# Optimization experiments

Measured on AMD Instinct MI355X. Metric: run time of the kernel, lower is better.

The kernel has to match this reference:

```python
import jax, jax.numpy as jnp
import numpy as np

D_MODEL = 512
N_HEAD = 8


def setup_inputs() -> dict:
    key = jax.random.key(0)
    ks = jax.random.split(key, 9)
    s = 1.0 / np.sqrt(D_MODEL)
    inp = {
        "x": jax.random.normal(ks[0], (2, 4096, D_MODEL), dtype=jnp.float32),
        "wq": jax.random.uniform(ks[1], (D_MODEL, D_MODEL), jnp.float32, -s, s),
        "bq": jax.random.uniform(ks[2], (D_MODEL,), jnp.float32, -s, s),
        "wk": jax.random.uniform(ks[3], (D_MODEL, D_MODEL), jnp.float32, -s, s),
        "bk": jax.random.uniform(ks[4], (D_MODEL,), jnp.float32, -s, s),
        "wv": jax.random.uniform(ks[5], (D_MODEL, D_MODEL), jnp.float32, -s, s),
        "bv": jax.random.uniform(ks[6], (D_MODEL,), jnp.float32, -s, s),
        "wo": jax.random.uniform(ks[7], (D_MODEL, D_MODEL), jnp.float32, -s, s),
        "bo": jax.random.uniform(ks[8], (D_MODEL,), jnp.float32, -s, s),
    }
    return inp


def reference(x, wq, bq, wk, bk, wv, bv, wo, bo):
    B, S, D = x.shape
    H = N_HEAD
    Dh = D // H

    def split_heads(t):  # [B,S,D] -> [B,H,S,Dh]
        return t.reshape(B, S, H, Dh).transpose(0, 2, 1, 3)

    q = split_heads(x @ wq.T + bq)
    k = split_heads(x @ wk.T + bk)
    v = split_heads(x @ wv.T + bv)

    # explicit (unfused) attention, matching the torch module
    score = jnp.einsum("bhsd,bhtd->bhst", q, k) / jnp.sqrt(jnp.float32(Dh))
    attn = jax.nn.softmax(score, axis=-1)
    out = jnp.einsum("bhst,bhtd->bhsd", attn, v)  # [B,H,S,Dh]

    out = out.transpose(0, 2, 1, 3).reshape(B, S, D)
    return out @ wo.T + bo
```

## Files before the change

### kernel.cpp

```cpp
#include <hip/hip_runtime.h>
#include <math.h>

#define S_LEN 4096
#define DMODEL 512
#define NHEAD 8
#define E_ELEMS ((size_t)8192 * 512)
#define QSCALE 0.18033688f

typedef __attribute__((ext_vector_type(8))) short bf16x8;
typedef __attribute__((ext_vector_type(4))) float f32x4;
typedef __attribute__((ext_vector_type(16))) float f32x16;
typedef unsigned short u16;
typedef unsigned int u32;

__device__ __forceinline__ u16 f2bf(float f) {
    u32 u = __float_as_uint(f);
    u += 0x7FFFu + ((u >> 16) & 1u);
    return (u16)(u >> 16);
}

#define MFMA16(a, b, c) __builtin_amdgcn_mfma_f32_16x16x32_bf16((a), (b), (c), 0, 0, 0)
#define MFMA32(a, b, c) __builtin_amdgcn_mfma_f32_32x32x16_bf16((a), (b), (c), 0, 0, 0)

__global__ __launch_bounds__(256) void cvt_x(const float* __restrict__ in,
                                             u16* __restrict__ out, int n4) {
    const int i = blockIdx.x * 256 + threadIdx.x;
    if (i >= n4) return;
    const float4 v = ((const float4*)in)[i];
    uint2 hp;
    hp.x = (u32)f2bf(v.x) | ((u32)f2bf(v.y) << 16);
    hp.y = (u32)f2bf(v.z) | ((u32)f2bf(v.w) << 16);
    ((uint2*)out)[i] = hp;
}

__global__ __launch_bounds__(256) void cvt_w(
    const float* __restrict__ wq, const float* __restrict__ wk,
    const float* __restrict__ wv, const float* __restrict__ wo,
    u16* __restrict__ oq, u16* __restrict__ ok,
    u16* __restrict__ ov, u16* __restrict__ oo) {
    const int i = blockIdx.x * 256 + threadIdx.x;
    {
        const float4 v = ((const float4*)wq)[i];
        uint2 hp;
        hp.x = (u32)f2bf(v.x * QSCALE) | ((u32)f2bf(v.y * QSCALE) << 16);
        hp.y = (u32)f2bf(v.z * QSCALE) | ((u32)f2bf(v.w * QSCALE) << 16);
        ((uint2*)oq)[i] = hp;
    }
    {
        const float4 v = ((const float4*)wk)[i];
        uint2 hp;
        hp.x = (u32)f2bf(v.x) | ((u32)f2bf(v.y) << 16);
        hp.y = (u32)f2bf(v.z) | ((u32)f2bf(v.w) << 16);
        ((uint2*)ok)[i] = hp;
    }
    {
        const float4 v = ((const float4*)wv)[i];
        uint2 hp;
        hp.x = (u32)f2bf(v.x) | ((u32)f2bf(v.y) << 16);
        hp.y = (u32)f2bf(v.z) | ((u32)f2bf(v.w) << 16);
        ((uint2*)ov)[i] = hp;
    }
    {
        const float4 v = ((const float4*)wo)[i];
        uint2 hp;
        hp.x = (u32)f2bf(v.x) | ((u32)f2bf(v.y) << 16);
        hp.y = (u32)f2bf(v.z) | ((u32)f2bf(v.w) << 16);
        ((uint2*)oo)[i] = hp;
    }
}

template<int MODE>
__global__ __launch_bounds__(256) void proj_kernel(
    const u16* __restrict__ Abf,
    const u16* __restrict__ Wq, const float* __restrict__ Bq,
    const u16* __restrict__ Wk, const float* __restrict__ Bk,
    const u16* __restrict__ Wv, const float* __restrict__ Bv,
    u16* __restrict__ Qo, u16* __restrict__ Ko, u16* __restrict__ Vt,
    float* __restrict__ Out)
{
    __shared__ __align__(16) u16 sm[18432];
    u16* Ah = sm;
    u16* Bh = sm + 9216;

    const int tid = threadIdx.x;
    const int w = tid >> 6, lane = tid & 63, g = lane >> 4, c = lane & 15;
    const int bm = blockIdx.x * 128;
    const int n0 = blockIdx.y * 64;
    const int z = (MODE == 0) ? blockIdx.z : 0;
    const u16* W   = (MODE == 1) ? Wq : (z == 0 ? Wq : (z == 1 ? Wk : Wv));
    const float* Bi = (MODE == 1) ? Bq : (z == 0 ? Bq : (z == 1 ? Bk : Bv));
    const float bsc = (MODE == 0 && z == 0) ? QSCALE : 1.0f;

    f32x4 acc[2][4];
    #pragma unroll
    for (int a = 0; a < 2; ++a)
        #pragma unroll
        for (int b = 0; b < 4; ++b) acc[a][b] = (f32x4){0.f, 0.f, 0.f, 0.f};

    #pragma unroll 1
    for (int kt = 0; kt < 8; ++kt) {
        const int k0 = kt * 64;
        __syncthreads();
        #pragma unroll
        for (int i = 0; i < 4; ++i) {
            const int slot = i * 256 + tid;
            const int r = slot >> 3, c8 = slot & 7;
            *(uint4*)(Ah + r * 72 + c8 * 8) =
                *(const uint4*)(Abf + (size_t)(bm + r) * DMODEL + k0 + c8 * 8);
        }
        #pragma unroll
        for (int i = 0; i < 2; ++i) {
            const int slot = i * 256 + tid;
            const int r = slot >> 3, c8 = slot & 7;
            *(uint4*)(Bh + r * 72 + c8 * 8) =
                *(const uint4*)(W + (size_t)(n0 + r) * DMODEL + k0 + c8 * 8);
        }
        __syncthreads();

        #pragma unroll
        for (int kc = 0; kc < 2; ++kc) {
            bf16x8 a[2], b[4];
            #pragma unroll
            for (int mf = 0; mf < 2; ++mf)
                a[mf] = *(const bf16x8*)(Ah + (w * 32 + mf * 16 + c) * 72 + kc * 32 + g * 8);
            #pragma unroll
            for (int nf = 0; nf < 4; ++nf)
                b[nf] = *(const bf16x8*)(Bh + (nf * 16 + c) * 72 + kc * 32 + g * 8);
            #pragma unroll
            for (int mf = 0; mf < 2; ++mf)
                #pragma unroll
                for (int nf = 0; nf < 4; ++nf)
                    acc[mf][nf] = MFMA16(a[mf], b[nf], acc[mf][nf]);
        }
    }

    if (MODE == 0 && z == 2) {
        __syncthreads();
        float* scr = (float*)sm;
        #pragma unroll
        for (int mf = 0; mf < 2; ++mf)
            #pragma unroll
            for (int nf = 0; nf < 4; ++nf) {
                const float bias = Bi[n0 + nf * 16 + c];
                #pragma unroll
                for (int r = 0; r < 4; ++r)
                    scr[(w * 32 + mf * 16 + 4 * g + r) * 72 + nf * 16 + c] =
                        acc[mf][nf][r] + bias;
            }
        __syncthreads();
        const int d = tid & 63, sb = tid >> 6;
        const int b = bm >> 12, h = n0 >> 6;
        const size_t obase =
            ((size_t)((b * NHEAD + h) * 64 + d)) * S_LEN + (bm & (S_LEN - 1)) + sb * 32;
        u16 th[32];
        #pragma unroll
        for (int j = 0; j < 32; ++j)
            th[j] = f2bf(scr[(sb * 32 + j) * 72 + d]);
        #pragma unroll
        for (int q = 0; q < 4; ++q)
            *(uint4*)(Vt + obase + q * 8) = *(const uint4*)&th[q * 8];
        return;
    }

    #pragma unroll
    for (int mf = 0; mf < 2; ++mf)
        #pragma unroll
        for (int nf = 0; nf < 4; ++nf) {
            const int n = n0 + nf * 16 + c;
            const float bias = Bi[n] * bsc;
            #pragma unroll
            for (int r = 0; r < 4; ++r) {
                const int m = bm + w * 32 + mf * 16 + 4 * g + r;
                const float v = acc[mf][nf][r] + bias;
                if (MODE == 1) {
                    Out[(size_t)m * DMODEL + n] = v;
                } else {
                    const int b = m >> 12, s = m & (S_LEN - 1);
                    const int hh = n >> 6, dd = n & 63;
                    const size_t o = ((size_t)((b * NHEAD + hh) * S_LEN + s)) * 64 + dd;
                    if (z == 0) Qo[o] = f2bf(v);
                    else        Ko[o] = f2bf(v);
                }
            }
        }
}

__global__ __launch_bounds__(256, 4) void attn_kernel(
    const u16* __restrict__ Qb, const u16* __restrict__ Kb,
    const u16* __restrict__ Vt, float* __restrict__ Op, float* __restrict__ Lp)
{
    __shared__ __align__(16) u16 sm[16384];

    const int tid = threadIdx.x;
    const int w = tid >> 6, l = tid & 63;
    const int r0 = l & 31, hi = l >> 5;

    const int f = blockIdx.x;
    const int wg = (f & 7) * 128 + (f >> 3);
    const int bh = wg >> 6, kvh = (wg >> 5) & 1, qb = wg & 31;
    const int b = bh >> 3, h = bh & 7;

    const size_t hoff = (size_t)bh * S_LEN * 64;
    const int qw = qb * 128 + w * 32;
    const int kv0 = kvh * 2048;

    bf16x8 qf[4];
    #pragma unroll
    for (int kc = 0; kc < 4; ++kc)
        qf[kc] = *(const bf16x8*)(Qb + hoff + (size_t)(qw + r0) * 64 + kc * 16 + hi * 8);

    const int rbase = r0 * 64;
    int soff[4];
    #pragma unroll
    for (int j = 0; j < 4; ++j) soff[j] = ((2 * j + hi) ^ (r0 & 7)) * 8;

    const int srow0 = w * 16 + (l >> 3);
    const int slot  = l & 7;
    const int srow1 = srow0 + 8;
    const u16* srcK0 = Kb + hoff + (size_t)(kv0 + srow0) * 64 + ((slot ^ (srow0 & 7)) * 8);
    const u16* srcK1 = Kb + hoff + (size_t)(kv0 + srow1) * 64 + ((slot ^ (srow1 & 7)) * 8);
    const u16* srcV0 = Vt + ((size_t)bh * 64 + srow0) * S_LEN + kv0 + ((slot ^ (srow0 & 7)) * 8);
    const u16* srcV1 = Vt + ((size_t)bh * 64 + srow1) * S_LEN + kv0 + ((slot ^ (srow1 & 7)) * 8);

#define STAGE(bufb, t) do {                                                        \
        u16* kb_ = sm + (bufb) * 8192 + w * 1024;                                  \
        u16* vb_ = kb_ + 4096;                                                     \
        __builtin_amdgcn_global_load_lds(srcK0 + (size_t)(t) * 4096, kb_,       16, 0, 0); \
        __builtin_amdgcn_global_load_lds(srcK1 + (size_t)(t) * 4096, kb_ + 512, 16, 0, 0); \
        __builtin_amdgcn_global_load_lds(srcV0 + (size_t)(t) * 64,   vb_,       16, 0, 0); \
        __builtin_amdgcn_global_load_lds(srcV1 + (size_t)(t) * 64,   vb_ + 512, 16, 0, 0); \
    } while (0)

    f32x16 o0 = {0.f,0.f,0.f,0.f,0.f,0.f,0.f,0.f,0.f,0.f,0.f,0.f,0.f,0.f,0.f,0.f};
    f32x16 o1 = {0.f,0.f,0.f,0.f,0.f,0.f,0.f,0.f,0.f,0.f,0.f,0.f,0.f,0.f,0.f,0.f};
    float lsum = 0.f;

    STAGE(0, 0);
    __syncthreads();
    int buf = 0;

    #pragma unroll 1
    for (int t = 0; t < 32; ++t) {
        if (t + 1 < 32) STAGE(buf ^ 1, t + 1);

        const u16* Kb_s = sm + buf * 8192;
        const u16* Vb_s = Kb_s + 4096;

        f32x16 s0 = {0.f,0.f,0.f,0.f,0.f,0.f,0.f,0.f,0.f,0.f,0.f,0.f,0.f,0.f,0.f,0.f};
        f32x16 s1 = {0.f,0.f,0.f,0.f,0.f,0.f,0.f,0.f,0.f,0.f,0.f,0.f,0.f,0.f,0.f,0.f};
        #pragma unroll
        for (int kc = 0; kc < 4; ++kc) {
            const bf16x8 k0 = *(const bf16x8*)(Kb_s + rbase + soff[kc]);
            const bf16x8 k1 = *(const bf16x8*)(Kb_s + 2048 + rbase + soff[kc]);
            s0 = MFMA32(k0, qf[kc], s0);
            s1 = MFMA32(k1, qf[kc], s1);
        }

        bf16x8 pa[4];
        #pragma unroll
        for (int kvf = 0; kvf < 2; ++kvf) {
            float pe[16];
            #pragma unroll
            for (int r = 0; r < 16; ++r) {
                const float sv = kvf ? s1[r] : s0[r];
                pe[r] = __builtin_amdgcn_exp2f(sv);
                lsum += pe[r];
            }
            #pragma unroll
            for (int hf = 0; hf < 2; ++hf) {
                const int rb = hf * 8;
                u32 x0, y0, x1, y1;
                asm("v_cvt_pk_bf16_f32 %0, %1, %2" : "=v"(x0) : "v"(pe[rb+0]), "v"(pe[rb+1]));
                asm("v_cvt_pk_bf16_f32 %0, %1, %2" : "=v"(y0) : "v"(pe[rb+4]), "v"(pe[rb+5]));
                asm("v_cvt_pk_bf16_f32 %0, %1, %2" : "=v"(x1) : "v"(pe[rb+2]), "v"(pe[rb+3]));
                asm("v_cvt_pk_bf16_f32 %0, %1, %2" : "=v"(y1) : "v"(pe[rb+6]), "v"(pe[rb+7]));
                asm volatile("v_permlane32_swap_b32 %0, %1" : "+v"(x0), "+v"(y0));
                asm volatile("v_permlane32_swap_b32 %0, %1" : "+v"(x1), "+v"(y1));
                union { u32 u[4]; bf16x8 v; } P;
                P.u[0] = x0; P.u[1] = x1; P.u[2] = y0; P.u[3] = y1;
                pa[kvf * 2 + hf] = P.v;
            }
        }

        #pragma unroll
        for (int kvc = 0; kvc < 4; ++kvc) {
            const bf16x8 v0 = *(const bf16x8*)(Vb_s + rbase + soff[kvc]);
            const bf16x8 v1 = *(const bf16x8*)(Vb_s + 2048 + rbase + soff[kvc]);
            o0 = MFMA32(pa[kvc], v0, o0);
            o1 = MFMA32(pa[kvc], v1, o1);
        }

        __syncthreads();
        buf ^= 1;
    }
#undef STAGE

    lsum += __shfl_xor(lsum, 32);
    if (hi == 0)
        Lp[((size_t)kvh * 16 + bh) * S_LEN + qw + r0] = lsum;

    float* Ob = Op + ((size_t)kvh * 8192 + (size_t)b * S_LEN) * DMODEL;
    #pragma unroll
    for (int df = 0; df < 2; ++df) {
        #pragma unroll
        for (int r = 0; r < 16; ++r) {
            const float ov = df ? o1[r] : o0[r];
            const int q = (r & 3) + 8 * (r >> 2) + 4 * hi;
            Ob[(size_t)(qw + q) * DMODEL + h * 64 + df * 32 + r0] = ov;
        }
    }
}

__global__ __launch_bounds__(256) void combine_kernel(
    const float* __restrict__ Op, const float* __restrict__ Lp,
    u16* __restrict__ A)
{
    const int i = blockIdx.x * 256 + threadIdx.x;
    const int m = i >> 6;
    const int col = (i & 63) * 8;
    const int b = m >> 12, s = m & (S_LEN - 1), h = col >> 6;
    const float l0 = Lp[((size_t)b * 8 + h) * S_LEN + s];
    const float l1 = Lp[(size_t)16 * S_LEN + ((size_t)b * 8 + h) * S_LEN + s];
    const float inv = 1.0f / (l0 + l1);
    const size_t base0 = (size_t)m * DMODEL + col;
    const size_t base1 = (size_t)8192 * DMODEL + base0;
    const float4 a0 = *(const float4*)(Op + base0);
    const float4 a1 = *(const float4*)(Op + base0 + 4);
    const float4 c0 = *(const float4*)(Op + base1);
    const float4 c1 = *(const float4*)(Op + base1 + 4);
    u16 r[8];
    r[0] = f2bf((a0.x + c0.x) * inv);
    r[1] = f2bf((a0.y + c0.y) * inv);
    r[2] = f2bf((a0.z + c0.z) * inv);
    r[3] = f2bf((a0.w + c0.w) * inv);
    r[4] = f2bf((a1.x + c1.x) * inv);
    r[5] = f2bf((a1.y + c1.y) * inv);
    r[6] = f2bf((a1.z + c1.z) * inv);
    r[7] = f2bf((a1.w + c1.w) * inv);
    *(uint4*)(A + base0) = *(const uint4*)r;
}

extern "C" void kernel_launch(void* const* d_in, const int* in_sizes, int n_in,
                              void* d_out, int out_size, void* d_ws, size_t ws_size,
                              hipStream_t stream)
{
    const float* x  = (const float*)d_in[0];
    const float* wq = (const float*)d_in[1];
    const float* bq = (const float*)d_in[2];
    const float* wk = (const float*)d_in[3];
    const float* bk = (const float*)d_in[4];
    const float* wv = (const float*)d_in[5];
    const float* bv = (const float*)d_in[6];
    const float* wo = (const float*)d_in[7];
    const float* bo = (const float*)d_in[8];

    u16* ws = (u16*)d_ws;
    const size_t E = E_ELEMS;
    u16* xbf  = ws;
    u16* Qbf  = ws + E;
    u16* Kbf  = ws + 2 * E;
    u16* Vtbf = ws + 3 * E;
    u16* wqbf = ws + 4 * E;
    u16* wkbf = wqbf + DMODEL * DMODEL;
    u16* wvbf = wkbf + DMODEL * DMODEL;
    u16* wobf = wvbf + DMODEL * DMODEL;
    float* Opart = (float*)(ws + 4 * E + 4 * DMODEL * DMODEL);
    float* Lpart = Opart + (size_t)2 * 8192 * DMODEL;

    cvt_x<<<dim3(4096), 256, 0, stream>>>(x, xbf, (int)(E / 4));
    cvt_w<<<dim3(256), 256, 0, stream>>>(wq, wk, wv, wo, wqbf, wkbf, wvbf, wobf);

    proj_kernel<0><<<dim3(64, 8, 3), 256, 0, stream>>>(
        xbf, wqbf, bq, wkbf, bk, wvbf, bv, Qbf, Kbf, Vtbf, nullptr);

    attn_kernel<<<dim3(1024), 256, 0, stream>>>(Qbf, Kbf, Vtbf, Opart, Lpart);

    combine_kernel<<<dim3(2048), 256, 0, stream>>>(Opart, Lpart, xbf);

    proj_kernel<1><<<dim3(64, 8, 1), 256, 0, stream>>>(
        xbf, wobf, bo, nullptr, nullptr, nullptr, nullptr,
        nullptr, nullptr, nullptr, (float*)d_out);
}
```

Measured before the change: 153.7 us.

## Fuse split-KV combine into attention and retile Q/K/O projections with direct LDS loads

```diff
diff --git a/kernel.cpp b/kernel.cpp
--- a/kernel.cpp
+++ b/kernel.cpp
@@ -70,32 +70,34 @@
 }
 
 template<int MODE>
-__global__ __launch_bounds__(256) void proj_kernel(
+__global__ __launch_bounds__(256) void proj2_kernel(
     const u16* __restrict__ Abf,
-    const u16* __restrict__ Wq, const float* __restrict__ Bq,
-    const u16* __restrict__ Wk, const float* __restrict__ Bk,
-    const u16* __restrict__ Wv, const float* __restrict__ Bv,
-    u16* __restrict__ Qo, u16* __restrict__ Ko, u16* __restrict__ Vt,
-    float* __restrict__ Out)
+    const u16* __restrict__ W0, const float* __restrict__ Bi0,
+    const u16* __restrict__ W1, const float* __restrict__ Bi1,
+    u16* __restrict__ Qo, u16* __restrict__ Ko, float* __restrict__ Out)
 {
-    __shared__ __align__(16) u16 sm[18432];
-    u16* Ah = sm;
-    u16* Bh = sm + 9216;
+    __shared__ __align__(16) u16 sm[16384];
+    u16* As = sm;
+    u16* Bs = sm + 8192;
 
     const int tid = threadIdx.x;
-    const int w = tid >> 6, lane = tid & 63, g = lane >> 4, c = lane & 15;
+    const int w = tid >> 6, l = tid & 63, g = (l >> 4), c = l & 15;
+    const int wr = w >> 1, wc = w & 1;
     const int bm = blockIdx.x * 128;
-    const int n0 = blockIdx.y * 64;
+    const int n0 = blockIdx.y * 128;
     const int z = (MODE == 0) ? blockIdx.z : 0;
-    const u16* W   = (MODE == 1) ? Wq : (z == 0 ? Wq : (z == 1 ? Wk : Wv));
-    const float* Bi = (MODE == 1) ? Bq : (z == 0 ? Bq : (z == 1 ? Bk : Bv));
+    const u16* W   = z ? W1 : W0;
+    const float* Bi = z ? Bi1 : Bi0;
     const float bsc = (MODE == 0 && z == 0) ? QSCALE : 1.0f;
 
-    f32x4 acc[2][4];
-    #pragma unroll
-    for (int a = 0; a < 2; ++a)
-        #pragma unroll
-        for (int b = 0; b < 4; ++b) acc[a][b] = (f32x4){0.f, 0.f, 0.f, 0.f};
+    const int sr = l >> 3;
+    const int slot = l & 7;
+
+    f32x4 acc[4][4];
+    #pragma unroll
+    for (int i = 0; i < 4; ++i)
+        #pragma unroll
+        for (int j = 0; j < 4; ++j) acc[i][j] = (f32x4){0.f, 0.f, 0.f, 0.f};
 
     #pragma unroll 1
     for (int kt = 0; kt < 8; ++kt) {
@@ -103,74 +105,47 @@
         __syncthreads();
         #pragma unroll
         for (int i = 0; i < 4; ++i) {
-            const int slot = i * 256 + tid;
-            const int r = slot >> 3, c8 = slot & 7;
-            *(uint4*)(Ah + r * 72 + c8 * 8) =
-                *(const uint4*)(Abf + (size_t)(bm + r) * DMODEL + k0 + c8 * 8);
-        }
-        #pragma unroll
-        for (int i = 0; i < 2; ++i) {
-            const int slot = i * 256 + tid;
-            const int r = slot >> 3, c8 = slot & 7;
-            *(uint4*)(Bh + r * 72 + c8 * 8) =
-                *(const uint4*)(W + (size_t)(n0 + r) * DMODEL + k0 + c8 * 8);
+            const int row = i * 32 + w * 8 + sr;
+            const int scol = (slot ^ (row & 7)) * 8;
+            __builtin_amdgcn_global_load_lds(
+                Abf + (size_t)(bm + row) * DMODEL + k0 + scol,
+                As + (i * 32 + w * 8) * 64, 16, 0, 0);
+            __builtin_amdgcn_global_load_lds(
+                W + (size_t)(n0 + row) * DMODEL + k0 + scol,
+                Bs + (i * 32 + w * 8) * 64, 16, 0, 0);
         }
         __syncthreads();
 
         #pragma unroll
         for (int kc = 0; kc < 2; ++kc) {
-            bf16x8 a[2], b[4];
-            #pragma unroll
-            for (int mf = 0; mf < 2; ++mf)
-                a[mf] = *(const bf16x8*)(Ah + (w * 32 + mf * 16 + c) * 72 + kc * 32 + g * 8);
-            #pragma unroll
-            for (int nf = 0; nf < 4; ++nf)
-                b[nf] = *(const bf16x8*)(Bh + (nf * 16 + c) * 72 + kc * 32 + g * 8);
-            #pragma unroll
-            for (int mf = 0; mf < 2; ++mf)
+            bf16x8 a[4], b[4];
+            #pragma unroll
+            for (int mf = 0; mf < 4; ++mf) {
+                const int ra = wr * 64 + mf * 16 + c;
+                a[mf] = *(const bf16x8*)(As + ra * 64 + (((kc * 4 + g) ^ (ra & 7)) * 8));
+            }
+            #pragma unroll
+            for (int nf = 0; nf < 4; ++nf) {
+                const int rb = wc * 64 + nf * 16 + c;
+                b[nf] = *(const bf16x8*)(Bs + rb * 64 + (((kc * 4 + g) ^ (rb & 7)) * 8));
+            }
+            #pragma unroll
+            for (int mf = 0; mf < 4; ++mf)
                 #pragma unroll
                 for (int nf = 0; nf < 4; ++nf)
                     acc[mf][nf] = MFMA16(a[mf], b[nf], acc[mf][nf]);
         }
     }
 
-    if (MODE == 0 && z == 2) {
-        __syncthreads();
-        float* scr = (float*)sm;
-        #pragma unroll
-        for (int mf = 0; mf < 2; ++mf)
-            #pragma unroll
-            for (int nf = 0; nf < 4; ++nf) {
-                const float bias = Bi[n0 + nf * 16 + c];
-                #pragma unroll
-                for (int r = 0; r < 4; ++r)
-                    scr[(w * 32 + mf * 16 + 4 * g + r) * 72 + nf * 16 + c] =
-                        acc[mf][nf][r] + bias;
-            }
-        __syncthreads();
-        const int d = tid & 63, sb = tid >> 6;
-        const int b = bm >> 12, h = n0 >> 6;
-        const size_t obase =
-            ((size_t)((b * NHEAD + h) * 64 + d)) * S_LEN + (bm & (S_LEN - 1)) + sb * 32;
-        u16 th[32];
-        #pragma unroll
-        for (int j = 0; j < 32; ++j)
-            th[j] = f2bf(scr[(sb * 32 + j) * 72 + d]);
-        #pragma unroll
-        for (int q = 0; q < 4; ++q)
-            *(uint4*)(Vt + obase + q * 8) = *(const uint4*)&th[q * 8];
-        return;
-    }
-
-    #pragma unroll
-    for (int mf = 0; mf < 2; ++mf)
+    #pragma unroll
+    for (int mf = 0; mf < 4; ++mf)
         #pragma unroll
         for (int nf = 0; nf < 4; ++nf) {
-            const int n = n0 + nf * 16 + c;
+            const int n = n0 + wc * 64 + nf * 16 + c;
             const float bias = Bi[n] * bsc;
             #pragma unroll
             for (int r = 0; r < 4; ++r) {
-                const int m = bm + w * 32 + mf * 16 + 4 * g + r;
+                const int m = bm + wr * 64 + mf * 16 + 4 * g + r;
                 const float v = acc[mf][nf][r] + bias;
                 if (MODE == 1) {
                     Out[(size_t)m * DMODEL + n] = v;
@@ -185,24 +160,107 @@
         }
 }
 
-__global__ __launch_bounds__(256, 4) void attn_kernel(
+__global__ __launch_bounds__(256) void proj_v_kernel(
+    const u16* __restrict__ Abf, const u16* __restrict__ Wv,
+    const float* __restrict__ Bv, u16* __restrict__ Vt)
+{
+    __shared__ __align__(16) u16 sm[18432];
+    u16* Ah = sm;
+    u16* Bh = sm + 9216;
+
+    const int tid = threadIdx.x;
+    const int w = tid >> 6, lane = tid & 63, g = lane >> 4, c = lane & 15;
+    const int bm = blockIdx.x * 128;
+    const int n0 = blockIdx.y * 64;
+
+    f32x4 acc[2][4];
+    #pragma unroll
+    for (int a = 0; a < 2; ++a)
+        #pragma unroll
+        for (int b = 0; b < 4; ++b) acc[a][b] = (f32x4){0.f, 0.f, 0.f, 0.f};
+
+    #pragma unroll 1
+    for (int kt = 0; kt < 8; ++kt) {
+        const int k0 = kt * 64;
+        __syncthreads();
+        #pragma unroll
+        for (int i = 0; i < 4; ++i) {
+            const int slot = i * 256 + tid;
+            const int r = slot >> 3, c8 = slot & 7;
+            *(uint4*)(Ah + r * 72 + c8 * 8) =
+                *(const uint4*)(Abf + (size_t)(bm + r) * DMODEL + k0 + c8 * 8);
+        }
+        #pragma unroll
+        for (int i = 0; i < 2; ++i) {
+            const int slot = i * 256 + tid;
+            const int r = slot >> 3, c8 = slot & 7;
+            *(uint4*)(Bh + r * 72 + c8 * 8) =
+                *(const uint4*)(Wv + (size_t)(n0 + r) * DMODEL + k0 + c8 * 8);
+        }
+        __syncthreads();
+
+        #pragma unroll
+        for (int kc = 0; kc < 2; ++kc) {
+            bf16x8 a[2], b[4];
+            #pragma unroll
+            for (int mf = 0; mf < 2; ++mf)
+                a[mf] = *(const bf16x8*)(Ah + (w * 32 + mf * 16 + c) * 72 + kc * 32 + g * 8);
+            #pragma unroll
+            for (int nf = 0; nf < 4; ++nf)
+                b[nf] = *(const bf16x8*)(Bh + (nf * 16 + c) * 72 + kc * 32 + g * 8);
+            #pragma unroll
+            for (int mf = 0; mf < 2; ++mf)
+                #pragma unroll
+                for (int nf = 0; nf < 4; ++nf)
+                    acc[mf][nf] = MFMA16(a[mf], b[nf], acc[mf][nf]);
+        }
+    }
+
+    __syncthreads();
+    float* scr = (float*)sm;
+    #pragma unroll
+    for (int mf = 0; mf < 2; ++mf)
+        #pragma unroll
+        for (int nf = 0; nf < 4; ++nf) {
+            const float bias = Bv[n0 + nf * 16 + c];
+            #pragma unroll
+            for (int r = 0; r < 4; ++r)
+                scr[(w * 32 + mf * 16 + 4 * g + r) * 72 + nf * 16 + c] =
+                    acc[mf][nf][r] + bias;
+        }
+    __syncthreads();
+    const int d = tid & 63, sb = tid >> 6;
+    const int b = bm >> 12, h = n0 >> 6;
+    const size_t obase =
+        ((size_t)((b * NHEAD + h) * 64 + d)) * S_LEN + (bm & (S_LEN - 1)) + sb * 32;
+    u16 th[32];
+    #pragma unroll
+    for (int j = 0; j < 32; ++j)
+        th[j] = f2bf(scr[(sb * 32 + j) * 72 + d]);
+    #pragma unroll
+    for (int q = 0; q < 4; ++q)
+        *(uint4*)(Vt + obase + q * 8) = *(const uint4*)&th[q * 8];
+}
+
+__global__ __launch_bounds__(512, 4) void attn_kernel(
     const u16* __restrict__ Qb, const u16* __restrict__ Kb,
-    const u16* __restrict__ Vt, float* __restrict__ Op, float* __restrict__ Lp)
+    const u16* __restrict__ Vt, u16* __restrict__ AO)
 {
-    __shared__ __align__(16) u16 sm[16384];
+    __shared__ __align__(16) u16 sm[32768];
 
     const int tid = threadIdx.x;
     const int w = tid >> 6, l = tid & 63;
+    const int kvg = w >> 2, wq = w & 3;
     const int r0 = l & 31, hi = l >> 5;
 
     const int f = blockIdx.x;
-    const int wg = (f & 7) * 128 + (f >> 3);
-    const int bh = wg >> 6, kvh = (wg >> 5) & 1, qb = wg & 31;
+    const int wg = (f & 7) * 64 + (f >> 3);
+    const int bh = wg >> 5, qb = wg & 31;
     const int b = bh >> 3, h = bh & 7;
 
     const size_t hoff = (size_t)bh * S_LEN * 64;
-    const int qw = qb * 128 + w * 32;
-    const int kv0 = kvh * 2048;
+    const int qw = qb * 128 + wq * 32;
+    const int kv0 = kvg * 2048;
 
     bf16x8 qf[4];
     #pragma unroll
@@ -214,7 +272,7 @@
     #pragma unroll
     for (int j = 0; j < 4; ++j) soff[j] = ((2 * j + hi) ^ (r0 & 7)) * 8;
 
-    const int srow0 = w * 16 + (l >> 3);
+    const int srow0 = wq * 16 + (l >> 3);
     const int slot  = l & 7;
     const int srow1 = srow0 + 8;
     const u16* srcK0 = Kb + hoff + (size_t)(kv0 + srow0) * 64 + ((slot ^ (srow0 & 7)) * 8);
@@ -222,8 +280,10 @@
     const u16* srcV0 = Vt + ((size_t)bh * 64 + srow0) * S_LEN + kv0 + ((slot ^ (srow0 & 7)) * 8);
     const u16* srcV1 = Vt + ((size_t)bh * 64 + srow1) * S_LEN + kv0 + ((slot ^ (srow1 & 7)) * 8);
 
+    u16* const grp = sm + kvg * 16384;
+
 #define STAGE(bufb, t) do {                                                        \
-        u16* kb_ = sm + (bufb) * 8192 + w * 1024;                                  \
+        u16* kb_ = grp + (bufb) * 8192 + wq * 1024;                                \
         u16* vb_ = kb_ + 4096;                                                     \
         __builtin_amdgcn_global_load_lds(srcK0 + (size_t)(t) * 4096, kb_,       16, 0, 0); \
         __builtin_amdgcn_global_load_lds(srcK1 + (size_t)(t) * 4096, kb_ + 512, 16, 0, 0); \
@@ -233,7 +293,7 @@
 
     f32x16 o0 = {0.f,0.f,0.f,0.f,0.f,0.f,0.f,0.f,0.f,0.f,0.f,0.f,0.f,0.f,0.f,0.f};
     f32x16 o1 = {0.f,0.f,0.f,0.f,0.f,0.f,0.f,0.f,0.f,0.f,0.f,0.f,0.f,0.f,0.f,0.f};
-    float lsum = 0.f;
+    f32x16 lacc = {0.f,0.f,0.f,0.f,0.f,0.f,0.f,0.f,0.f,0.f,0.f,0.f,0.f,0.f,0.f,0.f};
 
     STAGE(0, 0);
     __syncthreads();
@@ -243,11 +303,12 @@
     for (int t = 0; t < 32; ++t) {
         if (t + 1 < 32) STAGE(buf ^ 1, t + 1);
 
-        const u16* Kb_s = sm + buf * 8192;
+        const u16* Kb_s = grp + buf * 8192;
         const u16* Vb_s = Kb_s + 4096;
 
         f32x16 s0 = {0.f,0.f,0.f,0.f,0.f,0.f,0.f,0.f,0.f,0.f,0.f,0.f,0.f,0.f,0.f,0.f};
         f32x16 s1 = {0.f,0.f,0.f,0.f,0.f,0.f,0.f,0.f,0.f,0.f,0.f,0.f,0.f,0.f,0.f,0.f};
+        __builtin_amdgcn_s_setprio(1);
         #pragma unroll
         for (int kc = 0; kc < 4; ++kc) {
             const bf16x8 k0 = *(const bf16x8*)(Kb_s + rbase + soff[kc]);
@@ -255,25 +316,24 @@
             s0 = MFMA32(k0, qf[kc], s0);
             s1 = MFMA32(k1, qf[kc], s1);
         }
+        __builtin_amdgcn_s_setprio(0);
 
         bf16x8 pa[4];
         #pragma unroll
         for (int kvf = 0; kvf < 2; ++kvf) {
-            float pe[16];
-            #pragma unroll
-            for (int r = 0; r < 16; ++r) {
-                const float sv = kvf ? s1[r] : s0[r];
-                pe[r] = __builtin_amdgcn_exp2f(sv);
-                lsum += pe[r];
-            }
+            f32x16 pex;
+            #pragma unroll
+            for (int r = 0; r < 16; ++r)
+                pex[r] = __builtin_amdgcn_exp2f(kvf ? s1[r] : s0[r]);
+            lacc += pex;
             #pragma unroll
             for (int hf = 0; hf < 2; ++hf) {
                 const int rb = hf * 8;
                 u32 x0, y0, x1, y1;
-                asm("v_cvt_pk_bf16_f32 %0, %1, %2" : "=v"(x0) : "v"(pe[rb+0]), "v"(pe[rb+1]));
-                asm("v_cvt_pk_bf16_f32 %0, %1, %2" : "=v"(y0) : "v"(pe[rb+4]), "v"(pe[rb+5]));
-                asm("v_cvt_pk_bf16_f32 %0, %1, %2" : "=v"(x1) : "v"(pe[rb+2]), "v"(pe[rb+3]));
-                asm("v_cvt_pk_bf16_f32 %0, %1, %2" : "=v"(y1) : "v"(pe[rb+6]), "v"(pe[rb+7]));
+                asm("v_cvt_pk_bf16_f32 %0, %1, %2" : "=v"(x0) : "v"(pex[rb+0]), "v"(pex[rb+1]));
+                asm("v_cvt_pk_bf16_f32 %0, %1, %2" : "=v"(y0) : "v"(pex[rb+4]), "v"(pex[rb+5]));
+                asm("v_cvt_pk_bf16_f32 %0, %1, %2" : "=v"(x1) : "v"(pex[rb+2]), "v"(pex[rb+3]));
+                asm("v_cvt_pk_bf16_f32 %0, %1, %2" : "=v"(y1) : "v"(pex[rb+6]), "v"(pex[rb+7]));
                 asm volatile("v_permlane32_swap_b32 %0, %1" : "+v"(x0), "+v"(y0));
                 asm volatile("v_permlane32_swap_b32 %0, %1" : "+v"(x1), "+v"(y1));
                 union { u32 u[4]; bf16x8 v; } P;
@@ -282,6 +342,7 @@
             }
         }
 
+        __builtin_amdgcn_s_setprio(1);
         #pragma unroll
         for (int kvc = 0; kvc < 4; ++kvc) {
             const bf16x8 v0 = *(const bf16x8*)(Vb_s + rbase + soff[kvc]);
@@ -289,55 +350,42 @@
             o0 = MFMA32(pa[kvc], v0, o0);
             o1 = MFMA32(pa[kvc], v1, o1);
         }
+        __builtin_amdgcn_s_setprio(0);
 
         __syncthreads();
         buf ^= 1;
     }
 #undef STAGE
 
+    float lsum = 0.f;
+    #pragma unroll
+    for (int r = 0; r < 16; ++r) lsum += lacc[r];
     lsum += __shfl_xor(lsum, 32);
-    if (hi == 0)
-        Lp[((size_t)kvh * 16 + bh) * S_LEN + qw + r0] = lsum;
-
-    float* Ob = Op + ((size_t)kvh * 8192 + (size_t)b * S_LEN) * DMODEL;
-    #pragma unroll
-    for (int df = 0; df < 2; ++df) {
+
+    float* scrF = (float*)sm;
+    float* Lsh  = scrF + 8192;
+    if (hi == 0) Lsh[w * 32 + r0] = lsum;
+    if (kvg == 1) {
         #pragma unroll
         for (int r = 0; r < 16; ++r) {
-            const float ov = df ? o1[r] : o0[r];
             const int q = (r & 3) + 8 * (r >> 2) + 4 * hi;
-            Ob[(size_t)(qw + q) * DMODEL + h * 64 + df * 32 + r0] = ov;
-        }
-    }
-}
-
-__global__ __launch_bounds__(256) void combine_kernel(
-    const float* __restrict__ Op, const float* __restrict__ Lp,
-    u16* __restrict__ A)
-{
-    const int i = blockIdx.x * 256 + threadIdx.x;
-    const int m = i >> 6;
-    const int col = (i & 63) * 8;
-    const int b = m >> 12, s = m & (S_LEN - 1), h = col >> 6;
-    const float l0 = Lp[((size_t)b * 8 + h) * S_LEN + s];
-    const float l1 = Lp[(size_t)16 * S_LEN + ((size_t)b * 8 + h) * S_LEN + s];
-    const float inv = 1.0f / (l0 + l1);
-    const size_t base0 = (size_t)m * DMODEL + col;
-    const size_t base1 = (size_t)8192 * DMODEL + base0;
-    const float4 a0 = *(const float4*)(Op + base0);
-    const float4 a1 = *(const float4*)(Op + base0 + 4);
-    const float4 c0 = *(const float4*)(Op + base1);
-    const float4 c1 = *(const float4*)(Op + base1 + 4);
-    u16 r[8];
-    r[0] = f2bf((a0.x + c0.x) * inv);
-    r[1] = f2bf((a0.y + c0.y) * inv);
-    r[2] = f2bf((a0.z + c0.z) * inv);
-    r[3] = f2bf((a0.w + c0.w) * inv);
-    r[4] = f2bf((a1.x + c1.x) * inv);
-    r[5] = f2bf((a1.y + c1.y) * inv);
-    r[6] = f2bf((a1.z + c1.z) * inv);
-    r[7] = f2bf((a1.w + c1.w) * inv);
-    *(uint4*)(A + base0) = *(const uint4*)r;
+            scrF[wq * 2048 + q * 64 + r0]      = o0[r];
+            scrF[wq * 2048 + q * 64 + 32 + r0] = o1[r];
+        }
+    }
+    __syncthreads();
+    if (kvg == 0) {
+        #pragma unroll
+        for (int r = 0; r < 16; ++r) {
+            const int q = (r & 3) + 8 * (r >> 2) + 4 * hi;
+            const float L = Lsh[wq * 32 + q] + Lsh[(wq + 4) * 32 + q];
+            const float inv = 1.0f / L;
+            const int s = qw + q;
+            const size_t base = ((size_t)b * S_LEN + s) * DMODEL + h * 64;
+            AO[base + r0]      = f2bf((o0[r] + scrF[wq * 2048 + q * 64 + r0])      * inv);
+            AO[base + 32 + r0] = f2bf((o1[r] + scrF[wq * 2048 + q * 64 + 32 + r0]) * inv);
+        }
+    }
 }
 
 extern "C" void kernel_launch(void* const* d_in, const int* in_sizes, int n_in,
@@ -364,20 +412,17 @@
     u16* wkbf = wqbf + DMODEL * DMODEL;
     u16* wvbf = wkbf + DMODEL * DMODEL;
     u16* wobf = wvbf + DMODEL * DMODEL;
-    float* Opart = (float*)(ws + 4 * E + 4 * DMODEL * DMODEL);
-    float* Lpart = Opart + (size_t)2 * 8192 * DMODEL;
 
     cvt_x<<<dim3(4096), 256, 0, stream>>>(x, xbf, (int)(E / 4));
     cvt_w<<<dim3(256), 256, 0, stream>>>(wq, wk, wv, wo, wqbf, wkbf, wvbf, wobf);
 
-    proj_kernel<0><<<dim3(64, 8, 3), 256, 0, stream>>>(
-        xbf, wqbf, bq, wkbf, bk, wvbf, bv, Qbf, Kbf, Vtbf, nullptr);
-
-    attn_kernel<<<dim3(1024), 256, 0, stream>>>(Qbf, Kbf, Vtbf, Opart, Lpart);
-
-    combine_kernel<<<dim3(2048), 256, 0, stream>>>(Opart, Lpart, xbf);
-
-    proj_kernel<1><<<dim3(64, 8, 1), 256, 0, stream>>>(
-        xbf, wobf, bo, nullptr, nullptr, nullptr, nullptr,
-        nullptr, nullptr, nullptr, (float*)d_out);
-}
+    proj2_kernel<0><<<dim3(64, 4, 2), 256, 0, stream>>>(
+        xbf, wqbf, bq, wkbf, bk, Qbf, Kbf, nullptr);
+
+    proj_v_kernel<<<dim3(64, 8), 256, 0, stream>>>(xbf, wvbf, bv, Vtbf);
+
+    attn_kernel<<<dim3(512), 512, 0, stream>>>(Qbf, Kbf, Vtbf, xbf);
+
+    proj2_kernel<1><<<dim3(64, 4), 256, 0, stream>>>(
+        xbf, wobf, bo, nullptr, nullptr, nullptr, nullptr, (float*)d_out);
+}
```

Result: faster. 143.0 us (-7.0%).
